# Kernel optimization log

Hardware: AMD Instinct MI355X
Metric: run time of the kernel (lower is better)

The kernel has to match this reference:

```python
import jax, jax.numpy as jnp
import numpy as np

N = 20000          # nodes
DEG = 32           # avg degree / num_neighbors
E = N * DEG        # edges
D_IN = 64          # irreps_node_input dim
D_HID = 144        # irreps_node_hidden dim
D_OUT = 3          # irreps_node_out = 1x1o
D_SH = 9           # edge spherical harmonics, (lmax+1)^2
N_BASIS = 10       # number_of_basis
MUL = 64           # fc hidden width
ATTR = 4           # node_attr dim
NUM_NEIGHBORS = 32.0


def setup_inputs() -> dict:
    key = jax.random.key(0)
    ks = jax.random.split(key, 32)
    rn = lambda k, shape, scale: jax.random.normal(k, shape, jnp.float32) * scale
    inp = {}
    inp['x'] = rn(ks[0], (N, D_IN), 1.0)
    inp['node_attr'] = rn(ks[1], (N, ATTR), 1.0)
    inp['edge_attr'] = rn(ks[2], (E, D_SH), 1.0)
    inp['edge_length_embedding'] = jax.random.uniform(ks[3], (E, N_BASIS), jnp.float32)
    dims = [(D_IN, D_HID), (D_HID, D_HID), (D_HID, D_OUT)]
    i = 4
    for l, (di, do) in enumerate(dims):
        inp['A' + str(l)] = rn(ks[i], (di, do), di ** -0.5); i += 1
        inp['B' + str(l)] = rn(ks[i], (D_SH, do), D_SH ** -0.5); i += 1
        inp['W1_' + str(l)] = rn(ks[i], (N_BASIS, MUL), N_BASIS ** -0.5); i += 1
        inp['W2_' + str(l)] = rn(ks[i], (MUL, 2 * MUL), MUL ** -0.5); i += 1
        inp['W3_' + str(l)] = rn(ks[i], (2 * MUL, do), (2 * MUL) ** -0.5); i += 1
        inp['Wsc' + str(l)] = rn(ks[i], (di * ATTR, do), (di * ATTR) ** -0.5); i += 1
    inp['edge_src'] = jax.random.randint(ks[i], (E,), 0, N, jnp.int32); i += 1
    inp['edge_dst'] = jax.random.randint(ks[i], (E,), 0, N, jnp.int32)
    inp['batch'] = jnp.zeros((N,), jnp.int32)
    return inp


def _mp_layer(x, node_attr, sh, emb, src, dst, A, B, W1, W2, W3, Wsc):
    # One gather -> edge tensor-product (factorized, per-edge weights from
    # radial MLP) -> scatter layer, plus node_attr-modulated self-connection.
    n = x.shape[0]
    # radial weight network on edge length embedding: [E, d_out]
    gate = jax.nn.silu(jax.nn.silu(emb @ W1) @ W2) @ W3
    # factorized tensor product of gathered node feats with edge sph. harmonics
    msg = gate * (x[src] @ A) * (sh @ B)              # [E, d_out]
    agg = jax.ops.segment_sum(msg, dst, num_segments=n) / jnp.sqrt(NUM_NEIGHBORS)
    # self connection: tensor product of node features with node attributes
    sc = jnp.einsum('ni,nj->nij', x, node_attr).reshape(n, -1) @ Wsc  # [N, d_out]
    return sc + agg


def reference(x, node_attr, edge_attr, edge_length_embedding,
              A0, B0, W1_0, W2_0, W3_0, Wsc0,
              A1, B1, W1_1, W2_1, W3_1, Wsc1,
              A2, B2, W1_2, W2_2, W3_2, Wsc2,
              edge_src, edge_dst, batch):
    h = jax.nn.silu(_mp_layer(x, node_attr, edge_attr, edge_length_embedding,
                              edge_src, edge_dst, A0, B0, W1_0, W2_0, W3_0, Wsc0))
    h = jax.nn.silu(_mp_layer(h, node_attr, edge_attr, edge_length_embedding,
                              edge_src, edge_dst, A1, B1, W1_1, W2_1, W3_1, Wsc1))
    out = _mp_layer(h, node_attr, edge_attr, edge_length_embedding,
                    edge_src, edge_dst, A2, B2, W1_2, W2_2, W3_2, Wsc2)
    return out  # [N, 3]
```

## Files before the change

### kernel.cpp

```cpp
#include <hip/hip_runtime.h>
#include <hip/hip_bf16.h>

#define NN 20000
#define NE 640000
#define DSH 9
#define NB 10
#define ATTR 4

typedef __attribute__((ext_vector_type(8))) short bfrag8;
typedef __attribute__((ext_vector_type(4))) float f32x4;
typedef unsigned int u32;
typedef unsigned short u16;

constexpr float INV_SQRT_NB = 0.17677669529663687f;

__device__ __forceinline__ float silu_f(float x) {
    return x * __builtin_amdgcn_rcpf(1.0f + __expf(-x));
}

__device__ __forceinline__ u16 f2bf(float v) {
    union { __hip_bfloat16 h; u16 u; } c;
    c.h = __float2bfloat16(v);
    return c.u;
}

__device__ __forceinline__ f32x4 mfma16(bfrag8 a, bfrag8 b, f32x4 c) {
    return __builtin_amdgcn_mfma_f32_16x16x32_bf16(a, b, c, 0, 0, 0);
}

__global__ void count_k(const int* __restrict__ dst, int* __restrict__ cnt) {
    int i = blockIdx.x * blockDim.x + threadIdx.x;
    int st = gridDim.x * blockDim.x;
    for (; i < NE; i += st) atomicAdd(&cnt[dst[i]], 1);
}

__global__ void scan_k(const int* __restrict__ cnt, int* __restrict__ ptr) {
    __shared__ int ssum[256];
    const int T = 256, t = threadIdx.x;
    const int strip = (NN + T - 1) / T;
    int base = t * strip, s = 0;
    for (int i = 0; i < strip; i++) { int idx = base + i; if (idx < NN) s += cnt[idx]; }
    ssum[t] = s; __syncthreads();
    for (int off = 1; off < T; off <<= 1) {
        int v = (t >= off) ? ssum[t - off] : 0;
        __syncthreads();
        ssum[t] += v;
        __syncthreads();
    }
    int run = (t == 0) ? 0 : ssum[t - 1];
    for (int i = 0; i < strip; i++) {
        int idx = base + i;
        if (idx < NN) { int c = cnt[idx]; ptr[idx] = run; run += c; }
    }
    if (t == T - 1) ptr[NN] = run;
}

__global__ void fill_k(const int* __restrict__ dst, const int* __restrict__ ptr,
                       int* __restrict__ cnt, int* __restrict__ pos) {
    int i = blockIdx.x * blockDim.x + threadIdx.x;
    int st = gridDim.x * blockDim.x;
    for (; i < NE; i += st) {
        int d = dst[i];
        int r = atomicAdd(&cnt[d], 1);
        pos[i] = ptr[d] + r;
    }
}

__global__ void pack_bfrag(const float* __restrict__ W, u16* __restrict__ out,
                           int K, int N, int NT, int KS) {
    int tid = blockIdx.x * blockDim.x + threadIdx.x;
    if (tid >= NT * KS * 64) return;
    int l = tid & 63, ts = tid >> 6, s = ts % KS, t = ts / KS;
    int kb = s * 32 + ((l >> 4) << 3);
    int n = t * 16 + (l & 15);
    #pragma unroll
    for (int j = 0; j < 8; j++) {
        int k = kb + j;
        float v = (k < K && n < N) ? W[(size_t)k * N + n] : 0.f;
        out[(size_t)tid * 8 + j] = f2bf(v);
    }
}

template<int DI, int DO, int NT>
__global__ void node_prep(const float* __restrict__ xin,
                          const float* __restrict__ attr,
                          const float* __restrict__ A,
                          const float* __restrict__ Wsc,
                          float* __restrict__ xa,
                          float* __restrict__ agg)
{
    __shared__ float sx[NT][DI];
    __shared__ float sat[NT][ATTR];
    const int n0 = blockIdx.x * NT;
    for (int idx = threadIdx.x; idx < NT * DI; idx += blockDim.x)
        sx[idx / DI][idx % DI] = xin[(size_t)n0 * DI + idx];
    if (threadIdx.x < NT * ATTR)
        sat[threadIdx.x / ATTR][threadIdx.x % ATTR] = attr[(size_t)n0 * ATTR + threadIdx.x];
    __syncthreads();

    const int o = threadIdx.x;
    if (o < DO) {
        float at[NT][ATTR];
        #pragma unroll
        for (int n = 0; n < NT; n++) {
            at[n][0] = sat[n][0]; at[n][1] = sat[n][1];
            at[n][2] = sat[n][2]; at[n][3] = sat[n][3];
        }
        float accA[NT], accS[NT];
        #pragma unroll
        for (int n = 0; n < NT; n++) { accA[n] = 0.f; accS[n] = 0.f; }
        for (int i = 0; i < DI; i++) {
            float a  = A[(size_t)i * DO + o];
            float w0 = Wsc[(size_t)(i * 4 + 0) * DO + o];
            float w1 = Wsc[(size_t)(i * 4 + 1) * DO + o];
            float w2 = Wsc[(size_t)(i * 4 + 2) * DO + o];
            float w3 = Wsc[(size_t)(i * 4 + 3) * DO + o];
            #pragma unroll
            for (int n = 0; n < NT; n++) {
                float xi = sx[n][i];
                accA[n] = fmaf(xi, a, accA[n]);
                float s = fmaf(at[n][3], w3,
                          fmaf(at[n][2], w2,
                          fmaf(at[n][1], w1, at[n][0] * w0)));
                accS[n] = fmaf(xi, s, accS[n]);
            }
        }
        #pragma unroll
        for (int n = 0; n < NT; n++) {
            xa [(size_t)(n0 + n) * DO + o] = accA[n];
            agg[(size_t)(n0 + n) * DO + o] = accS[n];
        }
    }
}

#define T3STEP(T3)                                                             \
    {                                                                          \
        f32x4 shb = mfma16(a_sh, bff[(T3) * 64 + l], Z4);                      \
        f32x4 acc = mfma16(a_h2_0, w3f[((T3) * 4 + 0) * 64 + l], Z4);          \
        acc = mfma16(a_h2_1, w3f[((T3) * 4 + 1) * 64 + l], acc);               \
        acc = mfma16(a_h2_2, w3f[((T3) * 4 + 2) * 64 + l], acc);               \
        acc = mfma16(a_h2_3, w3f[((T3) * 4 + 3) * 64 + l], acc);               \
        const int n = (T3) * 16 + c;                                           \
        float v0 = acc[0] * shb[0] * xv[(T3) * 4 + 0] * INV_SQRT_NB;           \
        float v1 = acc[1] * shb[1] * xv[(T3) * 4 + 1] * INV_SQRT_NB;           \
        float v2 = acc[2] * shb[2] * xv[(T3) * 4 + 2] * INV_SQRT_NB;           \
        float v3 = acc[3] * shb[3] * xv[(T3) * 4 + 3] * INV_SQRT_NB;           \
        int m0 = g * 4;                                                        \
        int d0 = ((m0 + 0) * 96 + (n >> 1)) ^ (((m0 + 0) & 7) << 2);           \
        int d1 = ((m0 + 1) * 96 + (n >> 1)) ^ (((m0 + 1) & 7) << 2);           \
        int d2 = ((m0 + 2) * 96 + (n >> 1)) ^ (((m0 + 2) & 7) << 2);           \
        int d3 = ((m0 + 3) * 96 + (n >> 1)) ^ (((m0 + 3) & 7) << 2);           \
        ((u16*)(h2dw + d0))[n & 1] = f2bf(v0);                                 \
        ((u16*)(h2dw + d1))[n & 1] = f2bf(v1);                                 \
        ((u16*)(h2dw + d2))[n & 1] = f2bf(v2);                                 \
        ((u16*)(h2dw + d3))[n & 1] = f2bf(v3);                                 \
    }

template<int DO>
__global__ void __launch_bounds__(256)
edge_mfma(const float* __restrict__ emb, const float* __restrict__ sh,
          const int* __restrict__ src, const int* __restrict__ pos,
          const u16* __restrict__ W1f, const u16* __restrict__ W2f,
          const u16* __restrict__ W3f, const u16* __restrict__ Bf,
          const float* __restrict__ xa, u32* __restrict__ msgdw,
          float* __restrict__ msg3)
{
    __shared__ u32 ldsa[4 * 2400];
    const int wid = threadIdx.x >> 6;
    const int l   = threadIdx.x & 63;
    u32* Wl = ldsa + wid * 2400;
    float* embL  = (float*)Wl;
    float* shL   = (float*)(Wl + 160);
    int*   sidxL = (int*)(Wl + 304);
    int*   posL  = (int*)(Wl + 320);
    u32*   h1dw  = Wl + 352;
    u32*   h2dw  = Wl + 864;

    const bfrag8* w1f = (const bfrag8*)W1f;
    const bfrag8* w2f = (const bfrag8*)W2f;
    const bfrag8* w3f = (const bfrag8*)W3f;
    const bfrag8* bff = (const bfrag8*)Bf;

    const int g = l >> 4, c = l & 15;
    const int gwave = blockIdx.x * 4 + wid;
    const int nwave = gridDim.x * 4;
    const f32x4 Z4 = {0.f, 0.f, 0.f, 0.f};

    for (int it = gwave; it < NE / 16; it += nwave) {
        const int e0 = it * 16;
        {
            const float* ep = emb + (size_t)e0 * NB;
            for (int idx = l; idx < 16 * NB; idx += 64) embL[idx] = ep[idx];
            const float* sp = sh + (size_t)e0 * DSH;
            for (int idx = l; idx < 16 * DSH; idx += 64) shL[idx] = sp[idx];
            if (l < 16) { sidxL[l] = src[e0 + l]; posL[l] = pos[e0 + l]; }
        }
        const int si0 = sidxL[g * 4 + 0], si1 = sidxL[g * 4 + 1];
        const int si2 = sidxL[g * 4 + 2], si3 = sidxL[g * 4 + 3];
        float xv[(DO == 144) ? 36 : 1];
        if constexpr (DO == 144) {
            const float* xr0 = xa + (size_t)si0 * 144;
            const float* xr1 = xa + (size_t)si1 * 144;
            const float* xr2 = xa + (size_t)si2 * 144;
            const float* xr3 = xa + (size_t)si3 * 144;
            #pragma unroll
            for (int t3 = 0; t3 < 9; t3++) {
                xv[t3 * 4 + 0] = xr0[t3 * 16 + c];
                xv[t3 * 4 + 1] = xr1[t3 * 16 + c];
                xv[t3 * 4 + 2] = xr2[t3 * 16 + c];
                xv[t3 * 4 + 3] = xr3[t3 * 16 + c];
            }
        }
        bfrag8 a_emb;
        {
            const int kb = g << 3;
            #pragma unroll
            for (int j = 0; j < 8; j++) {
                int k = kb + j;
                float v = (k < NB) ? embL[c * NB + k] : 0.f;
                a_emb[j] = (short)f2bf(v);
            }
        }
        #pragma unroll
        for (int t = 0; t < 4; t++) {
            f32x4 acc = mfma16(a_emb, w1f[t * 64 + l], Z4);
            #pragma unroll
            for (int r = 0; r < 4; r++) {
                int m = g * 4 + r, n = t * 16 + c;
                int dw = (m * 32 + (n >> 1)) ^ ((m & 7) << 2);
                ((u16*)(h1dw + dw))[n & 1] = f2bf(silu_f(acc[r]));
            }
        }
        bfrag8 a_h1_0, a_h1_1;
        {
            int bb = c * 32 + g * 4, xr = (c & 7) << 2;
            a_h1_0 = *(const bfrag8*)(h1dw + ((bb +  0) ^ xr));
            a_h1_1 = *(const bfrag8*)(h1dw + ((bb + 16) ^ xr));
        }
        #pragma unroll
        for (int t2 = 0; t2 < 8; t2++) {
            f32x4 acc = mfma16(a_h1_0, w2f[(t2 * 2 + 0) * 64 + l], Z4);
            acc = mfma16(a_h1_1, w2f[(t2 * 2 + 1) * 64 + l], acc);
            #pragma unroll
            for (int r = 0; r < 4; r++) {
                int m = g * 4 + r, n = t2 * 16 + c;
                int dw = (m * 64 + (n >> 1)) ^ ((m & 7) << 2);
                ((u16*)(h2dw + dw))[n & 1] = f2bf(silu_f(acc[r]));
            }
        }
        bfrag8 a_h2_0, a_h2_1, a_h2_2, a_h2_3;
        {
            int bb = c * 64 + g * 4, xr = (c & 7) << 2;
            a_h2_0 = *(const bfrag8*)(h2dw + ((bb +  0) ^ xr));
            a_h2_1 = *(const bfrag8*)(h2dw + ((bb + 16) ^ xr));
            a_h2_2 = *(const bfrag8*)(h2dw + ((bb + 32) ^ xr));
            a_h2_3 = *(const bfrag8*)(h2dw + ((bb + 48) ^ xr));
        }
        bfrag8 a_sh;
        {
            const int kb = g << 3;
            #pragma unroll
            for (int j = 0; j < 8; j++) {
                int k = kb + j;
                float v = (k < DSH) ? shL[c * DSH + k] : 0.f;
                a_sh[j] = (short)f2bf(v);
            }
        }

        if constexpr (DO == 144) {
            T3STEP(0) T3STEP(1) T3STEP(2)
            __builtin_amdgcn_sched_barrier(0);
            T3STEP(3) T3STEP(4) T3STEP(5)
            __builtin_amdgcn_sched_barrier(0);
            T3STEP(6) T3STEP(7) T3STEP(8)
            for (int i = l; i < 1152; i += 64) {
                int m = i / 72;
                int xq = i - m * 72;
                u32 v = h2dw[(m * 96 + xq) ^ ((m & 7) << 2)];
                msgdw[(size_t)posL[m] * 72 + xq] = v;
            }
        } else {
            const int p0 = posL[g * 4 + 0], p1 = posL[g * 4 + 1];
            const int p2 = posL[g * 4 + 2], p3 = posL[g * 4 + 3];
            f32x4 shb = mfma16(a_sh, bff[l], Z4);
            f32x4 acc = mfma16(a_h2_0, w3f[0 * 64 + l], Z4);
            acc = mfma16(a_h2_1, w3f[1 * 64 + l], acc);
            acc = mfma16(a_h2_2, w3f[2 * 64 + l], acc);
            acc = mfma16(a_h2_3, w3f[3 * 64 + l], acc);
            if (c < 3) {
                msg3[(size_t)p0 * 3 + c] = acc[0] * shb[0] * xa[(size_t)si0 * 3 + c] * INV_SQRT_NB;
                msg3[(size_t)p1 * 3 + c] = acc[1] * shb[1] * xa[(size_t)si1 * 3 + c] * INV_SQRT_NB;
                msg3[(size_t)p2 * 3 + c] = acc[2] * shb[2] * xa[(size_t)si2 * 3 + c] * INV_SQRT_NB;
                msg3[(size_t)p3 * 3 + c] = acc[3] * shb[3] * xa[(size_t)si3 * 3 + c] * INV_SQRT_NB;
            }
        }
    }
}

template<int ACT>
__global__ void gather144(const u32* __restrict__ msgdw,
                          const int* __restrict__ ptr,
                          const float* __restrict__ sc,
                          float* __restrict__ outb)
{
    const int lane = threadIdx.x & 63;
    const int gw = blockIdx.x * (blockDim.x >> 6) + (threadIdx.x >> 6);
    const int nw = gridDim.x * (blockDim.x >> 6);
    for (int n = gw; n < NN; n += nw) {
        const int s0 = ptr[n], s1 = ptr[n + 1];
        float a0 = 0.f, a1 = 0.f, b0 = 0.f, b1 = 0.f;
        for (int s = s0; s < s1; s++) {
            u32 u = msgdw[(size_t)s * 72 + lane];
            a0 += __uint_as_float(u << 16);
            a1 += __uint_as_float(u & 0xffff0000u);
            if (lane < 8) {
                u32 v = msgdw[(size_t)s * 72 + 64 + lane];
                b0 += __uint_as_float(v << 16);
                b1 += __uint_as_float(v & 0xffff0000u);
            }
        }
        size_t base = (size_t)n * 144;
        float2 sv = *(const float2*)&sc[base + 2 * lane];
        float v0 = sv.x + a0, v1 = sv.y + a1;
        if (ACT) { v0 = silu_f(v0); v1 = silu_f(v1); }
        *(float2*)&outb[base + 2 * lane] = make_float2(v0, v1);
        if (lane < 8) {
            float2 sw = *(const float2*)&sc[base + 128 + 2 * lane];
            float w0 = sw.x + b0, w1 = sw.y + b1;
            if (ACT) { w0 = silu_f(w0); w1 = silu_f(w1); }
            *(float2*)&outb[base + 128 + 2 * lane] = make_float2(w0, w1);
        }
    }
}

__global__ void gather3(const float* __restrict__ msg3,
                        const int* __restrict__ ptr,
                        float* __restrict__ outb)
{
    int t = blockIdx.x * blockDim.x + threadIdx.x;
    if (t >= NN * 3) return;
    int n = t / 3, o = t - 3 * n;
    float a = 0.f;
    for (int s = ptr[n]; s < ptr[n + 1]; s++) a += msg3[(size_t)s * 3 + o];
    outb[t] += a;
}

extern "C" void kernel_launch(void* const* d_in, const int* in_sizes, int n_in,
                              void* d_out, int out_size, void* d_ws, size_t ws_size,
                              hipStream_t stream) {
    const float* x    = (const float*)d_in[0];
    const float* attr = (const float*)d_in[1];
    const float* sh   = (const float*)d_in[2];
    const float* emb  = (const float*)d_in[3];
    const float* A0   = (const float*)d_in[4];
    const float* B0   = (const float*)d_in[5];
    const float* W1_0 = (const float*)d_in[6];
    const float* W2_0 = (const float*)d_in[7];
    const float* W3_0 = (const float*)d_in[8];
    const float* Wsc0 = (const float*)d_in[9];
    const float* A1   = (const float*)d_in[10];
    const float* B1   = (const float*)d_in[11];
    const float* W1_1 = (const float*)d_in[12];
    const float* W2_1 = (const float*)d_in[13];
    const float* W3_1 = (const float*)d_in[14];
    const float* Wsc1 = (const float*)d_in[15];
    const float* A2   = (const float*)d_in[16];
    const float* B2   = (const float*)d_in[17];
    const float* W1_2 = (const float*)d_in[18];
    const float* W2_2 = (const float*)d_in[19];
    const float* W3_2 = (const float*)d_in[20];
    const float* Wsc2 = (const float*)d_in[21];
    const int*   src  = (const int*)d_in[22];
    const int*   dst  = (const int*)d_in[23];
    float* out = (float*)d_out;

    char* wp = (char*)d_ws;
    auto alloc = [&](size_t bytes) -> void* {
        void* r = (void*)wp;
        wp += (bytes + 255) & ~(size_t)255;
        return r;
    };
    float* xa   = (float*)alloc((size_t)NN * 144 * 4);
    float* agg  = (float*)alloc((size_t)NN * 144 * 4);
    float* hb0  = (float*)alloc((size_t)NN * 144 * 4);
    float* hb1  = (float*)alloc((size_t)NN * 144 * 4);
    int*   cnt  = (int*)alloc((size_t)NN * 4);
    int*   ptr  = (int*)alloc((size_t)(NN + 1) * 4);
    int*   pos  = (int*)alloc((size_t)NE * 4);
    u16* w1f0 = (u16*)alloc(4 * 64 * 8 * 2);
    u16* w2f0 = (u16*)alloc(16 * 64 * 8 * 2);
    u16* w3f0 = (u16*)alloc(36 * 64 * 8 * 2);
    u16* bf0  = (u16*)alloc(9 * 64 * 8 * 2);
    u16* w1f1 = (u16*)alloc(4 * 64 * 8 * 2);
    u16* w2f1 = (u16*)alloc(16 * 64 * 8 * 2);
    u16* w3f1 = (u16*)alloc(36 * 64 * 8 * 2);
    u16* bf1  = (u16*)alloc(9 * 64 * 8 * 2);
    u16* w1f2 = (u16*)alloc(4 * 64 * 8 * 2);
    u16* w2f2 = (u16*)alloc(16 * 64 * 8 * 2);
    u16* w3f2 = (u16*)alloc(4 * 64 * 8 * 2);
    u16* bf2  = (u16*)alloc(1 * 64 * 8 * 2);
    void* msgbuf = alloc((size_t)NE * 288);
    u32*   msgdw = (u32*)msgbuf;
    float* msg3  = (float*)msgbuf;

    hipMemsetAsync(cnt, 0, (size_t)NN * 4, stream);
    count_k<<<1024, 256, 0, stream>>>(dst, cnt);
    scan_k<<<1, 256, 0, stream>>>(cnt, ptr);
    hipMemsetAsync(cnt, 0, (size_t)NN * 4, stream);
    fill_k<<<1024, 256, 0, stream>>>(dst, ptr, cnt, pos);

    pack_bfrag<<<1, 256, 0, stream>>>(W1_0, w1f0, 10, 64, 4, 1);
    pack_bfrag<<<4, 256, 0, stream>>>(W2_0, w2f0, 64, 128, 8, 2);
    pack_bfrag<<<9, 256, 0, stream>>>(W3_0, w3f0, 128, 144, 9, 4);
    pack_bfrag<<<3, 256, 0, stream>>>(B0,   bf0,  9, 144, 9, 1);
    pack_bfrag<<<1, 256, 0, stream>>>(W1_1, w1f1, 10, 64, 4, 1);
    pack_bfrag<<<4, 256, 0, stream>>>(W2_1, w2f1, 64, 128, 8, 2);
    pack_bfrag<<<9, 256, 0, stream>>>(W3_1, w3f1, 128, 144, 9, 4);
    pack_bfrag<<<3, 256, 0, stream>>>(B1,   bf1,  9, 144, 9, 1);
    pack_bfrag<<<1, 256, 0, stream>>>(W1_2, w1f2, 10, 64, 4, 1);
    pack_bfrag<<<4, 256, 0, stream>>>(W2_2, w2f2, 64, 128, 8, 2);
    pack_bfrag<<<1, 256, 0, stream>>>(W3_2, w3f2, 128, 3, 1, 4);
    pack_bfrag<<<1, 256, 0, stream>>>(B2,   bf2,  9, 3, 1, 1);

    node_prep<64, 144, 8><<<NN / 8, 192, 0, stream>>>(x, attr, A0, Wsc0, xa, agg);
    edge_mfma<144><<<2500, 256, 0, stream>>>(emb, sh, src, pos, w1f0, w2f0, w3f0, bf0, xa, msgdw, nullptr);
    gather144<1><<<5000, 256, 0, stream>>>(msgdw, ptr, agg, hb0);

    node_prep<144, 144, 8><<<NN / 8, 192, 0, stream>>>(hb0, attr, A1, Wsc1, xa, agg);
    edge_mfma<144><<<2500, 256, 0, stream>>>(emb, sh, src, pos, w1f1, w2f1, w3f1, bf1, xa, msgdw, nullptr);
    gather144<1><<<5000, 256, 0, stream>>>(msgdw, ptr, agg, hb1);

    node_prep<144, 3, 8><<<NN / 8, 192, 0, stream>>>(hb1, attr, A2, Wsc2, xa, out);
    edge_mfma<3><<<2500, 256, 0, stream>>>(emb, sh, src, pos, w1f2, w2f2, w3f2, bf2, xa, nullptr, msg3);
    gather3<<<(NN * 3 + 255) / 256, 256, 0, stream>>>(msg3, ptr, out);
}
```

Before: 1.186 ms.

## Sort edges by source node to improve gather locality in edge kernels

```diff
diff --git a/kernel.cpp b/kernel.cpp
--- a/kernel.cpp
+++ b/kernel.cpp
@@ -28,10 +28,10 @@
     return __builtin_amdgcn_mfma_f32_16x16x32_bf16(a, b, c, 0, 0, 0);
 }
 
-__global__ void count_k(const int* __restrict__ dst, int* __restrict__ cnt) {
+__global__ void count_k(const int* __restrict__ idx, int* __restrict__ cnt) {
     int i = blockIdx.x * blockDim.x + threadIdx.x;
     int st = gridDim.x * blockDim.x;
-    for (; i < NE; i += st) atomicAdd(&cnt[dst[i]], 1);
+    for (; i < NE; i += st) atomicAdd(&cnt[idx[i]], 1);
 }
 
 __global__ void scan_k(const int* __restrict__ cnt, int* __restrict__ ptr) {
@@ -55,15 +55,32 @@
     if (t == T - 1) ptr[NN] = run;
 }
 
-__global__ void fill_k(const int* __restrict__ dst, const int* __restrict__ ptr,
+__global__ void fill_k(const int* __restrict__ idx, const int* __restrict__ ptr,
                        int* __restrict__ cnt, int* __restrict__ pos) {
     int i = blockIdx.x * blockDim.x + threadIdx.x;
     int st = gridDim.x * blockDim.x;
     for (; i < NE; i += st) {
-        int d = dst[i];
+        int d = idx[i];
         int r = atomicAdd(&cnt[d], 1);
         pos[i] = ptr[d] + r;
     }
+}
+
+__global__ void permute_edges(const float* __restrict__ emb, const float* __restrict__ sh,
+                              const int* __restrict__ src, const int* __restrict__ posD,
+                              const int* __restrict__ posS,
+                              float* __restrict__ embS, float* __restrict__ shS,
+                              int* __restrict__ srcS, int* __restrict__ posD2)
+{
+    int e = blockIdx.x * blockDim.x + threadIdx.x;
+    if (e >= NE) return;
+    int s = posS[e];
+    #pragma unroll
+    for (int k = 0; k < NB; k++)  embS[(size_t)s * NB + k] = emb[(size_t)e * NB + k];
+    #pragma unroll
+    for (int k = 0; k < DSH; k++) shS[(size_t)s * DSH + k] = sh[(size_t)e * DSH + k];
+    srcS[s]  = src[e];
+    posD2[s] = posD[e];
 }
 
 __global__ void pack_bfrag(const float* __restrict__ W, u16* __restrict__ out,
@@ -403,11 +420,33 @@
     u32*   msgdw = (u32*)msgbuf;
     float* msg3  = (float*)msgbuf;
 
+    int*   cntS  = (int*)alloc((size_t)NN * 4);
+    int*   ptrS  = (int*)alloc((size_t)(NN + 1) * 4);
+    int*   posS  = (int*)alloc((size_t)NE * 4);
+    float* embS  = (float*)alloc((size_t)NE * NB * 4);
+    float* shS   = (float*)alloc((size_t)NE * DSH * 4);
+    int*   srcS  = (int*)alloc((size_t)NE * 4);
+    int*   posD2 = (int*)alloc((size_t)NE * 4);
+    const bool sorted = ((size_t)(wp - (char*)d_ws) <= ws_size);
+
     hipMemsetAsync(cnt, 0, (size_t)NN * 4, stream);
     count_k<<<1024, 256, 0, stream>>>(dst, cnt);
     scan_k<<<1, 256, 0, stream>>>(cnt, ptr);
     hipMemsetAsync(cnt, 0, (size_t)NN * 4, stream);
     fill_k<<<1024, 256, 0, stream>>>(dst, ptr, cnt, pos);
+
+    const float* embU = emb;  const float* shU = sh;
+    const int*   srcU = src;  const int*   posU = pos;
+    if (sorted) {
+        hipMemsetAsync(cntS, 0, (size_t)NN * 4, stream);
+        count_k<<<1024, 256, 0, stream>>>(src, cntS);
+        scan_k<<<1, 256, 0, stream>>>(cntS, ptrS);
+        hipMemsetAsync(cntS, 0, (size_t)NN * 4, stream);
+        fill_k<<<1024, 256, 0, stream>>>(src, ptrS, cntS, posS);
+        permute_edges<<<(NE + 255) / 256, 256, 0, stream>>>(
+            emb, sh, src, pos, posS, embS, shS, srcS, posD2);
+        embU = embS; shU = shS; srcU = srcS; posU = posD2;
+    }
 
     pack_bfrag<<<1, 256, 0, stream>>>(W1_0, w1f0, 10, 64, 4, 1);
     pack_bfrag<<<4, 256, 0, stream>>>(W2_0, w2f0, 64, 128, 8, 2);
@@ -423,14 +462,14 @@
     pack_bfrag<<<1, 256, 0, stream>>>(B2,   bf2,  9, 3, 1, 1);
 
     node_prep<64, 144, 8><<<NN / 8, 192, 0, stream>>>(x, attr, A0, Wsc0, xa, agg);
-    edge_mfma<144><<<2500, 256, 0, stream>>>(emb, sh, src, pos, w1f0, w2f0, w3f0, bf0, xa, msgdw, nullptr);
+    edge_mfma<144><<<2500, 256, 0, stream>>>(embU, shU, srcU, posU, w1f0, w2f0, w3f0, bf0, xa, msgdw, nullptr);
     gather144<1><<<5000, 256, 0, stream>>>(msgdw, ptr, agg, hb0);
 
     node_prep<144, 144, 8><<<NN / 8, 192, 0, stream>>>(hb0, attr, A1, Wsc1, xa, agg);
-    edge_mfma<144><<<2500, 256, 0, stream>>>(emb, sh, src, pos, w1f1, w2f1, w3f1, bf1, xa, msgdw, nullptr);
+    edge_mfma<144><<<2500, 256, 0, stream>>>(embU, shU, srcU, posU, w1f1, w2f1, w3f1, bf1, xa, msgdw, nullptr);
     gather144<1><<<5000, 256, 0, stream>>>(msgdw, ptr, agg, hb1);
 
     node_prep<144, 3, 8><<<NN / 8, 192, 0, stream>>>(hb1, attr, A2, Wsc2, xa, out);
-    edge_mfma<3><<<2500, 256, 0, stream>>>(emb, sh, src, pos, w1f2, w2f2, w3f2, bf2, xa, nullptr, msg3);
+    edge_mfma<3><<<2500, 256, 0, stream>>>(embU, shU, srcU, posU, w1f2, w2f2, w3f2, bf2, xa, nullptr, msg3);
     gather3<<<(NN * 3 + 255) / 256, 256, 0, stream>>>(msg3, ptr, out);
 }
```

Result: no change. 1.195 ms (+0.7%).
